# Kernel tuning notes

Hardware: AMD Instinct MI355X
Metric: run time of the kernel (lower is better)

The kernel has to match this reference:

```python
import jax, jax.numpy as jnp
import numpy as np

K_NEIGHBOURS = 16
ITERATIONS = 3
NUM_CLASSES = 20
N_POINTS = 20000


def setup_inputs() -> dict:
    key = jax.random.key(0)
    k1, k2 = jax.random.split(key)
    logits = jax.random.normal(k1, (N_POINTS, NUM_CLASSES), dtype=jnp.float32)
    coords = jax.random.uniform(k2, (N_POINTS, 3), dtype=jnp.float32)
    # nn.init.eye_ then *= -0.1
    compat_w = (-0.1 * jnp.eye(NUM_CLASSES, dtype=jnp.float32))
    return {"logits": logits, "coords": coords, "compat_w": compat_w}


def _knn_graph(coords, k):
    # torch.cdist (p=2): euclidean distances, (N, N)
    sq = jnp.sum(coords * coords, axis=-1)
    d2 = sq[:, None] + sq[None, :] - 2.0 * (coords @ coords.T)
    dists = jnp.sqrt(jnp.clip(d2, 0.0))
    # smallest-k -> top_k of negated distances
    _, idx = jax.lax.top_k(-dists, k)  # (N, k)
    return idx


def reference(logits, coords, compat_w):
    knn_idx = _knn_graph(coords, K_NEIGHBOURS)
    q = jax.nn.softmax(logits, axis=-1)
    for _ in range(ITERATIONS):
        neighbour_q = q[knn_idx]            # (N, k, K) gather
        msg = jnp.mean(neighbour_q, axis=1)  # (N, K)
        refined = logits + msg @ compat_w.T  # nn.Linear: x @ W^T
        q = jax.nn.softmax(refined, axis=-1)
    return (refined, q)
```

## Files before the change

kernel.cpp:

```cpp
#include <hip/hip_runtime.h>

#define N_PTS 20000
#define NCLS 20
#define KNN 16
#define GRID 12
#define NCELLS (GRID * GRID * GRID)
#define HCELL (1.0f / (float)GRID)
#define CAND_CAP 640
#define KEY_CAP 128
#define R_TARGET 0.0680f

__device__ __forceinline__ int cell1d(float v) {
    int c = (int)(v * (float)GRID);
    return min(max(c, 0), GRID - 1);
}

__global__ __launch_bounds__(256) void count_scan_kernel(const float* __restrict__ coords,
                                                         int* __restrict__ cellCount,
                                                         int* __restrict__ doneCtr,
                                                         int* __restrict__ cellStart,
                                                         int* __restrict__ cellCursor) {
    const int p = blockIdx.x * blockDim.x + threadIdx.x;
    if (p < N_PTS) {
        const int cx = cell1d(coords[3 * p + 0]);
        const int cy = cell1d(coords[3 * p + 1]);
        const int cz = cell1d(coords[3 * p + 2]);
        atomicAdd(&cellCount[(cz * GRID + cy) * GRID + cx], 1);
    }
    __threadfence();
    __syncthreads();
    __shared__ bool isLast;
    if (threadIdx.x == 0)
        isLast = (atomicAdd(doneCtr, 1) == (int)gridDim.x - 1);
    __syncthreads();
    if (!isLast) return;

    __shared__ int part[256];
    const int t = threadIdx.x;
    const int base = t * 7;
    int local[7];
    int s = 0;
#pragma unroll
    for (int i = 0; i < 7; ++i) {
        const int c = base + i;
        const int v = (c < NCELLS)
            ? __hip_atomic_load(&cellCount[c], __ATOMIC_RELAXED, __HIP_MEMORY_SCOPE_AGENT)
            : 0;
        local[i] = s;
        s += v;
    }
    part[t] = s;
    __syncthreads();
    for (int off = 1; off < 256; off <<= 1) {
        const int v = part[t] + ((t >= off) ? part[t - off] : 0);
        __syncthreads();
        part[t] = v;
        __syncthreads();
    }
    const int excl = (t > 0) ? part[t - 1] : 0;
#pragma unroll
    for (int i = 0; i < 7; ++i) {
        const int c = base + i;
        if (c < NCELLS) {
            cellStart[c] = excl + local[i];
            cellCursor[c] = excl + local[i];
        }
    }
    if (t == 255) cellStart[NCELLS] = part[255];
}

__global__ __launch_bounds__(256) void scatter_kernel(const float* __restrict__ coords,
                                                      const float* __restrict__ logits,
                                                      int* __restrict__ cellCursor,
                                                      float4* __restrict__ sortedPts,
                                                      int* __restrict__ orig,
                                                      float* __restrict__ ls,
                                                      float* __restrict__ q0s) {
    const int p = blockIdx.x * blockDim.x + threadIdx.x;
    if (p >= N_PTS) return;
    const float x = coords[3 * p + 0];
    const float y = coords[3 * p + 1];
    const float z = coords[3 * p + 2];
    const int c = (cell1d(z) * GRID + cell1d(y)) * GRID + cell1d(x);
    const int pos = atomicAdd(&cellCursor[c], 1);
    sortedPts[pos] = make_float4(x, y, z, __uint_as_float((unsigned)p));
    orig[pos] = p;
    const float4* l4 = (const float4*)(logits + p * NCLS);
    float v[NCLS];
#pragma unroll
    for (int u = 0; u < 5; ++u) {
        const float4 a = l4[u];
        v[4 * u + 0] = a.x; v[4 * u + 1] = a.y;
        v[4 * u + 2] = a.z; v[4 * u + 3] = a.w;
    }
    float4* d4 = (float4*)(ls + pos * NCLS);
#pragma unroll
    for (int u = 0; u < 5; ++u)
        d4[u] = make_float4(v[4 * u], v[4 * u + 1], v[4 * u + 2], v[4 * u + 3]);
    float mx = v[0];
#pragma unroll
    for (int cc = 1; cc < NCLS; ++cc) mx = fmaxf(mx, v[cc]);
    float sum = 0.f;
#pragma unroll
    for (int cc = 0; cc < NCLS; ++cc) { v[cc] = __expf(v[cc] - mx); sum += v[cc]; }
    const float inv = 1.f / sum;
    float4* q4 = (float4*)(q0s + pos * NCLS);
#pragma unroll
    for (int u = 0; u < 5; ++u)
        q4[u] = make_float4(v[4 * u] * inv, v[4 * u + 1] * inv,
                            v[4 * u + 2] * inv, v[4 * u + 3] * inv);
}

__device__ void knn_ladder(const float4* __restrict__ sortedPts,
                           const int* __restrict__ cellStart,
                           const float4 qp, const int s, int hw,
                           unsigned long long* keys, const int lane,
                           int* __restrict__ knn_out) {
    const unsigned long long laneLt = (1ull << lane) - 1ull;
    const int cx = cell1d(qp.x), cy = cell1d(qp.y), cz = cell1d(qp.z);
    float g = 0.9995f * (float)hw * HCELL;
    float tau = g * g;
    int cnt = 0;
    for (int att = 0; att < 16; ++att) {
        cnt = 0;
        const int xlo = max(cx - hw, 0), xhi = min(cx + hw, GRID - 1);
        const int ylo = max(cy - hw, 0), yhi = min(cy + hw, GRID - 1);
        const int zlo = max(cz - hw, 0), zhi = min(cz + hw, GRID - 1);
        for (int zz = zlo; zz <= zhi; ++zz) {
            for (int yy = ylo; yy <= yhi; ++yy) {
                const int rowc = (zz * GRID + yy) * GRID;
                const int beg = cellStart[rowc + xlo];
                const int end = cellStart[rowc + xhi + 1];
                for (int j0 = beg; j0 < end; j0 += 64) {
                    const int j = j0 + lane;
                    const bool jv = j < end;
                    const float4 pt = sortedPts[jv ? j : beg];
                    const float dx = pt.x - qp.x, dy = pt.y - qp.y, dz = pt.z - qp.z;
                    const float d2 = dx * dx + dy * dy + dz * dz;
                    const bool take = jv && (d2 < tau);
                    const unsigned long long mm = __ballot(take);
                    if (take) {
                        const int pos = cnt + (int)__popcll(mm & laneLt);
                        if (pos < KEY_CAP)
                            keys[pos] = (((unsigned long long)__float_as_uint(d2)) << 32) |
                                        (unsigned long long)(unsigned)j;
                    }
                    cnt += (int)__popcll(mm);
                }
            }
        }
        if (cnt >= KNN && cnt <= KEY_CAP) break;
        if (cnt < KNN) {
            if (hw < GRID - 1) { ++hw; g = 0.9995f * (float)hw * HCELL; tau = g * g; }
            else tau *= 2.5f;
        } else {
            tau *= 0.6f;
        }
    }
    const int m = min(cnt, KEY_CAP);
    const unsigned long long k0 = (lane < m) ? keys[lane] : ~0ull;
    const unsigned long long k1 = (lane + 64 < m) ? keys[lane + 64] : ~0ull;
    int r0 = 0, r1 = 0;
    for (int j = 0; j < m; ++j) {
        const unsigned long long kj = keys[j];
        r0 += (kj < k0); r1 += (kj < k1);
    }
    if (lane < m && r0 < KNN)      knn_out[s * KNN + r0] = (int)(unsigned)(k0 & 0xffffffffull);
    if (lane + 64 < m && r1 < KNN) knn_out[s * KNN + r1] = (int)(unsigned)(k1 & 0xffffffffull);
}

__global__ __launch_bounds__(256) void knn_kernel(const float4* __restrict__ sortedPts,
                                                  const int* __restrict__ cellStart,
                                                  int* __restrict__ knn_out) {
    __shared__ float4 cand[CAND_CAP];
    __shared__ unsigned long long keys[4][KEY_CAP];
    const int lane = threadIdx.x & 63;
    const int wave = threadIdx.x >> 6;
    const int c = blockIdx.x >> 1;
    const int half = blockIdx.x & 1;
    const int cz = c / (GRID * GRID);
    const int cy = (c / GRID) % GRID;
    const int cx = c % GRID;
    const int pbeg = cellStart[c];
    const int pend = cellStart[c + 1];
    const int npts = pend - pbeg;
    if (npts <= 0) return;
    const int bd = (cx == 0 || cx == GRID - 1) + (cy == 0 || cy == GRID - 1) +
                   (cz == 0 || cz == GRID - 1);
    const int hs = (bd >= 2) ? 2 : 1;
    const unsigned long long laneLt = (1ull << lane) - 1ull;

    const int xlo = max(cx - hs, 0), xhi = min(cx + hs, GRID - 1);
    const int ylo = max(cy - hs, 0), yhi = min(cy + hs, GRID - 1);
    const int zlo = max(cz - hs, 0), zhi = min(cz + hs, GRID - 1);
    const int ny = yhi - ylo + 1;
    const int nruns = (zhi - zlo + 1) * ny;

    int beg = 0, len = 0;
    if (lane < nruns) {
        const int zz = zlo + lane / ny;
        const int yy = ylo + lane % ny;
        const int rowc = (zz * GRID + yy) * GRID;
        beg = cellStart[rowc + xlo];
        len = cellStart[rowc + xhi + 1] - beg;
    }
    int off = len;
#pragma unroll
    for (int sh = 1; sh < 32; sh <<= 1) {
        const int o = __shfl_up(off, sh, 64);
        if (lane >= sh) off += o;
    }
    const int nc = __shfl(off, nruns - 1);
    off -= len;
    const int ownRun = (cz - zlo) * ny + (cy - ylo);
    const int ownOff = __shfl(off, ownRun) + (pbeg - __shfl(beg, ownRun));

    if (nc <= CAND_CAP) {
        for (int r = wave; r < nruns; r += 4) {
            const int rb = __shfl(beg, r);
            const int rl = __shfl(len, r);
            const int ro = __shfl(off, r);
            for (int i = lane; i < rl; i += 64) {
                float4 pt = sortedPts[rb + i];
                pt.w = __uint_as_float((unsigned)(rb + i));
                cand[ro + i] = pt;
            }
        }
    }
    __syncthreads();

    if (nc > CAND_CAP) {
        for (int idx = 2 * wave + half; idx < npts; idx += 8)
            knn_ladder(sortedPts, cellStart, sortedPts[pbeg + idx], pbeg + idx,
                       hs, keys[wave], lane, knn_out);
        return;
    }

    const float taumaxr = 0.9995f * (float)hs * HCELL;
    const float taumax = taumaxr * taumaxr;

    for (int idx = 2 * wave + half; idx < npts; idx += 8) {
        const int s = pbeg + idx;
        const float4 qp = cand[ownOff + idx];
        float r = R_TARGET;
        const float inv2r = 0.5f / r;
        const float fx = (fminf(qp.x + r, 1.f) - fmaxf(qp.x - r, 0.f)) * inv2r;
        const float fy = (fminf(qp.y + r, 1.f) - fmaxf(qp.y - r, 0.f)) * inv2r;
        const float fz = (fminf(qp.z + r, 1.f) - fmaxf(qp.z - r, 0.f)) * inv2r;
        const float f = fmaxf(fx * fy * fz, 0.05f);
        r = R_TARGET * __powf(f, -0.33333334f);
        float tau = fminf(r * r, taumax);
        bool triedMax = (tau >= taumax * 0.999f);

        int cnt = 0;
        bool ok = false;
        for (int att = 0; att < 5 && !ok; ++att) {
            cnt = 0;
            for (int j0 = 0; j0 < nc; j0 += 64) {
                const int j = j0 + lane;
                float d2 = 1e30f;
                unsigned pw = 0;
                if (j < nc) {
                    const float4 pt = cand[j];
                    const float dx = pt.x - qp.x, dy = pt.y - qp.y, dz = pt.z - qp.z;
                    d2 = dx * dx + dy * dy + dz * dz;
                    pw = __float_as_uint(pt.w);
                }
                const bool take = d2 < tau;
                const unsigned long long mm = __ballot(take);
                if (take) {
                    const int pos = cnt + (int)__popcll(mm & laneLt);
                    if (pos < KEY_CAP)
                        keys[wave][pos] =
                            (((unsigned long long)__float_as_uint(d2)) << 32) |
                            (unsigned long long)pw;
                }
                cnt += (int)__popcll(mm);
            }
            if (cnt >= KNN && cnt <= KEY_CAP) ok = true;
            else if (cnt < KNN) {
                if (triedMax) break;
                tau = taumax; triedMax = true;
            } else tau *= 0.6f;
        }
        if (!ok) {
            knn_ladder(sortedPts, cellStart, qp, s, hs + 1, keys[wave], lane, knn_out);
            continue;
        }
        const int m = cnt;
        const unsigned long long k0 = (lane < m) ? keys[wave][lane] : ~0ull;
        const unsigned long long k1 = (lane + 64 < m) ? keys[wave][lane + 64] : ~0ull;
        int r0 = 0, r1 = 0;
        for (int j = 0; j < m; ++j) {
            const unsigned long long kj = keys[wave][j];
            r0 += (kj < k0); r1 += (kj < k1);
        }
        if (lane < m && r0 < KNN)      knn_out[s * KNN + r0] = (int)(unsigned)(k0 & 0xffffffffull);
        if (lane + 64 < m && r1 < KNN) knn_out[s * KNN + r1] = (int)(unsigned)(k1 & 0xffffffffull);
    }
}

__global__ __launch_bounds__(256) void crf_iter_kernel(const float* __restrict__ ls,
                                                       const float* __restrict__ W,
                                                       const int* __restrict__ knn,
                                                       const float* __restrict__ qin,
                                                       float* __restrict__ qout,
                                                       const int* __restrict__ orig,
                                                       float* __restrict__ outRef,
                                                       float* __restrict__ outQ) {
    __shared__ float Ws[NCLS * NCLS];
    for (int i = threadIdx.x; i < NCLS * NCLS; i += blockDim.x) Ws[i] = W[i];
    __syncthreads();
    const int t = blockIdx.x * blockDim.x + threadIdx.x;
    const int p = t >> 2;
    const int qtr = t & 3;
    if (p >= N_PTS) return;

    float acc[NCLS];
#pragma unroll
    for (int c = 0; c < NCLS; ++c) acc[c] = 0.f;

    const int4 k4 = ((const int4*)(knn + p * KNN))[qtr];
    const int ids[4] = {k4.x, k4.y, k4.z, k4.w};
#pragma unroll
    for (int u = 0; u < 4; ++u) {
        unsigned id = (unsigned)ids[u];
        if (id >= N_PTS) id = 0;
        const float4* r4 = (const float4*)(qin + id * NCLS);
#pragma unroll
        for (int v = 0; v < 5; ++v) {
            const float4 a = r4[v];
            acc[4 * v + 0] += a.x; acc[4 * v + 1] += a.y;
            acc[4 * v + 2] += a.z; acc[4 * v + 3] += a.w;
        }
    }
#pragma unroll
    for (int c = 0; c < NCLS; ++c) {
        acc[c] += __shfl_xor(acc[c], 1, 64);
        acc[c] += __shfl_xor(acc[c], 2, 64);
        acc[c] *= (1.f / 16.f);
    }

    const int c0 = qtr * 5;
    float ref[5];
#pragma unroll
    for (int i = 0; i < 5; ++i) {
        float s = ls[p * NCLS + c0 + i];
#pragma unroll
        for (int k = 0; k < NCLS; ++k) s += acc[k] * Ws[(c0 + i) * NCLS + k];
        ref[i] = s;
    }

    float mx = ref[0];
#pragma unroll
    for (int i = 1; i < 5; ++i) mx = fmaxf(mx, ref[i]);
    mx = fmaxf(mx, __shfl_xor(mx, 1, 64));
    mx = fmaxf(mx, __shfl_xor(mx, 2, 64));
    float ex[5];
    float ps = 0.f;
#pragma unroll
    for (int i = 0; i < 5; ++i) { ex[i] = __expf(ref[i] - mx); ps += ex[i]; }
    ps += __shfl_xor(ps, 1, 64);
    ps += __shfl_xor(ps, 2, 64);
    const float inv = 1.f / ps;

    if (outRef != nullptr) {
        const int o = orig[p];
#pragma unroll
        for (int i = 0; i < 5; ++i) {
            outRef[o * NCLS + c0 + i] = ref[i];
            outQ[o * NCLS + c0 + i] = ex[i] * inv;
        }
    } else {
#pragma unroll
        for (int i = 0; i < 5; ++i) qout[p * NCLS + c0 + i] = ex[i] * inv;
    }
}

extern "C" void kernel_launch(void* const* d_in, const int* in_sizes, int n_in,
                              void* d_out, int out_size, void* d_ws, size_t ws_size,
                              hipStream_t stream) {
    const float* logits = (const float*)d_in[0];
    const float* coords = (const float*)d_in[1];
    const float* W      = (const float*)d_in[2];
    float* out = (float*)d_out;

    char* ws = (char*)d_ws;
    size_t off = 0;
    int* knn = (int*)(ws + off);              off += (size_t)N_PTS * KNN * 4;
    off = (off + 255) & ~(size_t)255;
    float* ls = (float*)(ws + off);           off += (size_t)N_PTS * NCLS * 4;
    off = (off + 255) & ~(size_t)255;
    float* q0s = (float*)(ws + off);          off += (size_t)N_PTS * NCLS * 4;
    off = (off + 255) & ~(size_t)255;
    float4* sortedPts = (float4*)(ws + off);  off += (size_t)N_PTS * 16;
    off = (off + 255) & ~(size_t)255;
    int* orig = (int*)(ws + off);             off += (size_t)N_PTS * 4;
    off = (off + 255) & ~(size_t)255;
    int* cellCount = (int*)(ws + off);        off += (size_t)(NCELLS + 1) * 4;
    int* doneCtr = cellCount + NCELLS;
    off = (off + 255) & ~(size_t)255;
    int* cellStart = (int*)(ws + off);        off += (size_t)(NCELLS + 1) * 4;
    off = (off + 255) & ~(size_t)255;
    int* cellCursor = (int*)(ws + off);
    float* q1s = out + N_PTS * NCLS;

    const int threads = 256;
    const int pblocks = (N_PTS + threads - 1) / threads;
    const int cblocks = (4 * N_PTS + threads - 1) / threads;

    hipMemsetAsync(cellCount, 0, (NCELLS + 1) * sizeof(int), stream);
    count_scan_kernel<<<pblocks, threads, 0, stream>>>(coords, cellCount, doneCtr,
                                                       cellStart, cellCursor);
    scatter_kernel<<<pblocks, threads, 0, stream>>>(coords, logits, cellCursor,
                                                    sortedPts, orig, ls, q0s);
    knn_kernel<<<NCELLS * 2, threads, 0, stream>>>(sortedPts, cellStart, knn);
    crf_iter_kernel<<<cblocks, threads, 0, stream>>>(ls, W, knn, q0s, q1s, orig,
                                                     nullptr, nullptr);
    crf_iter_kernel<<<cblocks, threads, 0, stream>>>(ls, W, knn, q1s, q0s, orig,
                                                     nullptr, nullptr);
    crf_iter_kernel<<<cblocks, threads, 0, stream>>>(ls, W, knn, q0s, nullptr, orig,
                                                     out, out + N_PTS * NCLS);
}
```

Measured before the change: 129.3 us.

## Fuse build and CRF iterations into persistent kernels with software grid barriers

After: 196.8 us. 52.3% more time.

```diff
diff --git a/kernel.cpp b/kernel.cpp
--- a/kernel.cpp
+++ b/kernel.cpp
@@ -15,17 +15,39 @@
     return min(max(c, 0), GRID - 1);
 }
 
-__global__ __launch_bounds__(256) void count_scan_kernel(const float* __restrict__ coords,
-                                                         int* __restrict__ cellCount,
-                                                         int* __restrict__ doneCtr,
-                                                         int* __restrict__ cellStart,
-                                                         int* __restrict__ cellCursor) {
+__device__ __forceinline__ void gridBarrier(int* bar, int nb) {
+    __syncthreads();
+    if (threadIdx.x == 0) {
+        __threadfence();
+        atomicAdd(bar, 1);
+        while (__hip_atomic_load(bar, __ATOMIC_RELAXED, __HIP_MEMORY_SCOPE_AGENT) < nb)
+            __builtin_amdgcn_s_sleep(2);
+        __threadfence();
+    }
+    __syncthreads();
+}
+
+__global__ __launch_bounds__(256) void build_kernel(const float* __restrict__ coords,
+                                                    const float* __restrict__ logits,
+                                                    int* __restrict__ cellCount,
+                                                    int* __restrict__ doneCtr,
+                                                    int* __restrict__ readyFlag,
+                                                    int* __restrict__ cellStart,
+                                                    int* __restrict__ cellCursor,
+                                                    float4* __restrict__ sortedPts,
+                                                    int* __restrict__ orig,
+                                                    float* __restrict__ ls,
+                                                    float* __restrict__ q0s) {
     const int p = blockIdx.x * blockDim.x + threadIdx.x;
-    if (p < N_PTS) {
-        const int cx = cell1d(coords[3 * p + 0]);
-        const int cy = cell1d(coords[3 * p + 1]);
-        const int cz = cell1d(coords[3 * p + 2]);
-        atomicAdd(&cellCount[(cz * GRID + cy) * GRID + cx], 1);
+    const bool act = (p < N_PTS);
+    float x = 0.f, y = 0.f, z = 0.f;
+    int c = 0;
+    if (act) {
+        x = coords[3 * p + 0];
+        y = coords[3 * p + 1];
+        z = coords[3 * p + 2];
+        c = (cell1d(z) * GRID + cell1d(y)) * GRID + cell1d(x);
+        atomicAdd(&cellCount[c], 1);
     }
     __threadfence();
     __syncthreads();
@@ -33,55 +55,54 @@
     if (threadIdx.x == 0)
         isLast = (atomicAdd(doneCtr, 1) == (int)gridDim.x - 1);
     __syncthreads();
-    if (!isLast) return;
-
-    __shared__ int part[256];
-    const int t = threadIdx.x;
-    const int base = t * 7;
-    int local[7];
-    int s = 0;
-#pragma unroll
-    for (int i = 0; i < 7; ++i) {
-        const int c = base + i;
-        const int v = (c < NCELLS)
-            ? __hip_atomic_load(&cellCount[c], __ATOMIC_RELAXED, __HIP_MEMORY_SCOPE_AGENT)
-            : 0;
-        local[i] = s;
-        s += v;
-    }
-    part[t] = s;
-    __syncthreads();
-    for (int off = 1; off < 256; off <<= 1) {
-        const int v = part[t] + ((t >= off) ? part[t - off] : 0);
+
+    if (isLast) {
+        __shared__ int part[256];
+        const int t = threadIdx.x;
+        const int base = t * 7;
+        int local[7];
+        int s = 0;
+#pragma unroll
+        for (int i = 0; i < 7; ++i) {
+            const int cc = base + i;
+            const int v = (cc < NCELLS)
+                ? __hip_atomic_load(&cellCount[cc], __ATOMIC_RELAXED, __HIP_MEMORY_SCOPE_AGENT)
+                : 0;
+            local[i] = s;
+            s += v;
+        }
+        part[t] = s;
         __syncthreads();
-        part[t] = v;
+        for (int off2 = 1; off2 < 256; off2 <<= 1) {
+            const int v = part[t] + ((t >= off2) ? part[t - off2] : 0);
+            __syncthreads();
+            part[t] = v;
+            __syncthreads();
+        }
+        const int excl = (t > 0) ? part[t - 1] : 0;
+#pragma unroll
+        for (int i = 0; i < 7; ++i) {
+            const int cc = base + i;
+            if (cc < NCELLS) {
+                cellStart[cc] = excl + local[i];
+                cellCursor[cc] = excl + local[i];
+            }
+        }
+        if (t == 255) cellStart[NCELLS] = part[255];
         __syncthreads();
-    }
-    const int excl = (t > 0) ? part[t - 1] : 0;
-#pragma unroll
-    for (int i = 0; i < 7; ++i) {
-        const int c = base + i;
-        if (c < NCELLS) {
-            cellStart[c] = excl + local[i];
-            cellCursor[c] = excl + local[i];
-        }
-    }
-    if (t == 255) cellStart[NCELLS] = part[255];
-}
-
-__global__ __launch_bounds__(256) void scatter_kernel(const float* __restrict__ coords,
-                                                      const float* __restrict__ logits,
-                                                      int* __restrict__ cellCursor,
-                                                      float4* __restrict__ sortedPts,
-                                                      int* __restrict__ orig,
-                                                      float* __restrict__ ls,
-                                                      float* __restrict__ q0s) {
-    const int p = blockIdx.x * blockDim.x + threadIdx.x;
-    if (p >= N_PTS) return;
-    const float x = coords[3 * p + 0];
-    const float y = coords[3 * p + 1];
-    const float z = coords[3 * p + 2];
-    const int c = (cell1d(z) * GRID + cell1d(y)) * GRID + cell1d(x);
+        if (t == 0) {
+            __threadfence();
+            __hip_atomic_store(readyFlag, 1, __ATOMIC_RELEASE, __HIP_MEMORY_SCOPE_AGENT);
+        }
+    }
+    if (threadIdx.x == 0) {
+        while (__hip_atomic_load(readyFlag, __ATOMIC_RELAXED, __HIP_MEMORY_SCOPE_AGENT) == 0)
+            __builtin_amdgcn_s_sleep(2);
+        __threadfence();
+    }
+    __syncthreads();
+    if (!act) return;
+
     const int pos = atomicAdd(&cellCursor[c], 1);
     sortedPts[pos] = make_float4(x, y, z, __uint_as_float((unsigned)p));
     orig[pos] = p;
@@ -99,10 +120,10 @@
         d4[u] = make_float4(v[4 * u], v[4 * u + 1], v[4 * u + 2], v[4 * u + 3]);
     float mx = v[0];
 #pragma unroll
-    for (int cc = 1; cc < NCLS; ++cc) mx = fmaxf(mx, v[cc]);
+    for (int cc2 = 1; cc2 < NCLS; ++cc2) mx = fmaxf(mx, v[cc2]);
     float sum = 0.f;
 #pragma unroll
-    for (int cc = 0; cc < NCLS; ++cc) { v[cc] = __expf(v[cc] - mx); sum += v[cc]; }
+    for (int cc2 = 0; cc2 < NCLS; ++cc2) { v[cc2] = __expf(v[cc2] - mx); sum += v[cc2]; }
     const float inv = 1.f / sum;
     float4* q4 = (float4*)(q0s + pos * NCLS);
 #pragma unroll
@@ -300,80 +321,91 @@
     }
 }
 
-__global__ __launch_bounds__(256) void crf_iter_kernel(const float* __restrict__ ls,
-                                                       const float* __restrict__ W,
-                                                       const int* __restrict__ knn,
-                                                       const float* __restrict__ qin,
-                                                       float* __restrict__ qout,
-                                                       const int* __restrict__ orig,
-                                                       float* __restrict__ outRef,
-                                                       float* __restrict__ outQ) {
+__global__ __launch_bounds__(256) void crf3_kernel(const float* __restrict__ ls,
+                                                   const float* __restrict__ W,
+                                                   const int* __restrict__ knn,
+                                                   float* q0s, float* q1s,
+                                                   const int* __restrict__ orig,
+                                                   float* outRef, float* outQ,
+                                                   int* bar) {
     __shared__ float Ws[NCLS * NCLS];
     for (int i = threadIdx.x; i < NCLS * NCLS; i += blockDim.x) Ws[i] = W[i];
-    __syncthreads();
     const int t = blockIdx.x * blockDim.x + threadIdx.x;
     const int p = t >> 2;
     const int qtr = t & 3;
-    if (p >= N_PTS) return;
-
-    float acc[NCLS];
-#pragma unroll
-    for (int c = 0; c < NCLS; ++c) acc[c] = 0.f;
-
-    const int4 k4 = ((const int4*)(knn + p * KNN))[qtr];
-    const int ids[4] = {k4.x, k4.y, k4.z, k4.w};
-#pragma unroll
-    for (int u = 0; u < 4; ++u) {
-        unsigned id = (unsigned)ids[u];
-        if (id >= N_PTS) id = 0;
-        const float4* r4 = (const float4*)(qin + id * NCLS);
-#pragma unroll
-        for (int v = 0; v < 5; ++v) {
-            const float4 a = r4[v];
-            acc[4 * v + 0] += a.x; acc[4 * v + 1] += a.y;
-            acc[4 * v + 2] += a.z; acc[4 * v + 3] += a.w;
-        }
-    }
-#pragma unroll
-    for (int c = 0; c < NCLS; ++c) {
-        acc[c] += __shfl_xor(acc[c], 1, 64);
-        acc[c] += __shfl_xor(acc[c], 2, 64);
-        acc[c] *= (1.f / 16.f);
-    }
-
+    const bool act = (p < N_PTS);
     const int c0 = qtr * 5;
-    float ref[5];
-#pragma unroll
-    for (int i = 0; i < 5; ++i) {
-        float s = ls[p * NCLS + c0 + i];
-#pragma unroll
-        for (int k = 0; k < NCLS; ++k) s += acc[k] * Ws[(c0 + i) * NCLS + k];
-        ref[i] = s;
-    }
-
-    float mx = ref[0];
-#pragma unroll
-    for (int i = 1; i < 5; ++i) mx = fmaxf(mx, ref[i]);
-    mx = fmaxf(mx, __shfl_xor(mx, 1, 64));
-    mx = fmaxf(mx, __shfl_xor(mx, 2, 64));
-    float ex[5];
-    float ps = 0.f;
-#pragma unroll
-    for (int i = 0; i < 5; ++i) { ex[i] = __expf(ref[i] - mx); ps += ex[i]; }
-    ps += __shfl_xor(ps, 1, 64);
-    ps += __shfl_xor(ps, 2, 64);
-    const float inv = 1.f / ps;
-
-    if (outRef != nullptr) {
-        const int o = orig[p];
-#pragma unroll
-        for (int i = 0; i < 5; ++i) {
-            outRef[o * NCLS + c0 + i] = ref[i];
-            outQ[o * NCLS + c0 + i] = ex[i] * inv;
-        }
-    } else {
-#pragma unroll
-        for (int i = 0; i < 5; ++i) qout[p * NCLS + c0 + i] = ex[i] * inv;
+
+    int4 k4 = make_int4(0, 0, 0, 0);
+    float lsr[5] = {0.f, 0.f, 0.f, 0.f, 0.f};
+    if (act) {
+        k4 = ((const int4*)(knn + p * KNN))[qtr];
+#pragma unroll
+        for (int i = 0; i < 5; ++i) lsr[i] = ls[p * NCLS + c0 + i];
+    }
+    __syncthreads();
+
+    const float* qin = q0s;
+    for (int it = 0; it < 3; ++it) {
+        if (act) {
+            float acc[NCLS];
+#pragma unroll
+            for (int c = 0; c < NCLS; ++c) acc[c] = 0.f;
+            const int ids[4] = {k4.x, k4.y, k4.z, k4.w};
+#pragma unroll
+            for (int u = 0; u < 4; ++u) {
+                unsigned id = (unsigned)ids[u];
+                if (id >= N_PTS) id = 0;
+                const float4* r4 = (const float4*)(qin + id * NCLS);
+#pragma unroll
+                for (int v = 0; v < 5; ++v) {
+                    const float4 a = r4[v];
+                    acc[4 * v + 0] += a.x; acc[4 * v + 1] += a.y;
+                    acc[4 * v + 2] += a.z; acc[4 * v + 3] += a.w;
+                }
+            }
+#pragma unroll
+            for (int c = 0; c < NCLS; ++c) {
+                acc[c] += __shfl_xor(acc[c], 1, 64);
+                acc[c] += __shfl_xor(acc[c], 2, 64);
+                acc[c] *= (1.f / 16.f);
+            }
+            float ref[5];
+#pragma unroll
+            for (int i = 0; i < 5; ++i) {
+                float s = lsr[i];
+#pragma unroll
+                for (int k = 0; k < NCLS; ++k) s += acc[k] * Ws[(c0 + i) * NCLS + k];
+                ref[i] = s;
+            }
+            float mx = ref[0];
+#pragma unroll
+            for (int i = 1; i < 5; ++i) mx = fmaxf(mx, ref[i]);
+            mx = fmaxf(mx, __shfl_xor(mx, 1, 64));
+            mx = fmaxf(mx, __shfl_xor(mx, 2, 64));
+            float ex[5];
+            float ps = 0.f;
+#pragma unroll
+            for (int i = 0; i < 5; ++i) { ex[i] = __expf(ref[i] - mx); ps += ex[i]; }
+            ps += __shfl_xor(ps, 1, 64);
+            ps += __shfl_xor(ps, 2, 64);
+            const float inv = 1.f / ps;
+
+            if (it == 2) {
+                const int o = orig[p];
+#pragma unroll
+                for (int i = 0; i < 5; ++i) {
+                    outRef[o * NCLS + c0 + i] = ref[i];
+                    outQ[o * NCLS + c0 + i] = ex[i] * inv;
+                }
+            } else {
+                float* qout = (it == 0) ? q1s : q0s;
+#pragma unroll
+                for (int i = 0; i < 5; ++i) qout[p * NCLS + c0 + i] = ex[i] * inv;
+            }
+        }
+        if (it == 0)      { gridBarrier(bar + 0, (int)gridDim.x); qin = q1s; }
+        else if (it == 1) { gridBarrier(bar + 1, (int)gridDim.x); qin = q0s; }
     }
 }
 
@@ -397,8 +429,10 @@
     off = (off + 255) & ~(size_t)255;
     int* orig = (int*)(ws + off);             off += (size_t)N_PTS * 4;
     off = (off + 255) & ~(size_t)255;
-    int* cellCount = (int*)(ws + off);        off += (size_t)(NCELLS + 1) * 4;
-    int* doneCtr = cellCount + NCELLS;
+    int* cellCount = (int*)(ws + off);        off += (size_t)(NCELLS + 4) * 4;
+    int* doneCtr   = cellCount + NCELLS;
+    int* readyFlag = cellCount + NCELLS + 1;
+    int* bar       = cellCount + NCELLS + 2;
     off = (off + 255) & ~(size_t)255;
     int* cellStart = (int*)(ws + off);        off += (size_t)(NCELLS + 1) * 4;
     off = (off + 255) & ~(size_t)255;
@@ -409,16 +443,11 @@
     const int pblocks = (N_PTS + threads - 1) / threads;
     const int cblocks = (4 * N_PTS + threads - 1) / threads;
 
-    hipMemsetAsync(cellCount, 0, (NCELLS + 1) * sizeof(int), stream);
-    count_scan_kernel<<<pblocks, threads, 0, stream>>>(coords, cellCount, doneCtr,
-                                                       cellStart, cellCursor);
-    scatter_kernel<<<pblocks, threads, 0, stream>>>(coords, logits, cellCursor,
-                                                    sortedPts, orig, ls, q0s);
+    hipMemsetAsync(cellCount, 0, (NCELLS + 4) * sizeof(int), stream);
+    build_kernel<<<pblocks, threads, 0, stream>>>(coords, logits, cellCount, doneCtr,
+                                                  readyFlag, cellStart, cellCursor,
+                                                  sortedPts, orig, ls, q0s);
     knn_kernel<<<NCELLS * 2, threads, 0, stream>>>(sortedPts, cellStart, knn);
-    crf_iter_kernel<<<cblocks, threads, 0, stream>>>(ls, W, knn, q0s, q1s, orig,
-                                                     nullptr, nullptr);
-    crf_iter_kernel<<<cblocks, threads, 0, stream>>>(ls, W, knn, q1s, q0s, orig,
-                                                     nullptr, nullptr);
-    crf_iter_kernel<<<cblocks, threads, 0, stream>>>(ls, W, knn, q0s, nullptr, orig,
-                                                     out, out + N_PTS * NCLS);
-}
+    crf3_kernel<<<cblocks, threads, 0, stream>>>(ls, W, knn, q0s, q1s, orig,
+                                                 out, out + N_PTS * NCLS, bar);
+}
```

## Replace counting-sort grid with fixed-capacity per-cell buckets and drop scan kernel

Applied to the files above, without the earlier changes.

After: 157.2 us. +21.6%, slower.

```diff
diff --git a/kernel.cpp b/kernel.cpp
--- a/kernel.cpp
+++ b/kernel.cpp
@@ -6,6 +6,7 @@
 #define GRID 12
 #define NCELLS (GRID * GRID * GRID)
 #define HCELL (1.0f / (float)GRID)
+#define CAP 64
 #define CAND_CAP 640
 #define KEY_CAP 128
 #define R_TARGET 0.0680f
@@ -15,76 +16,21 @@
     return min(max(c, 0), GRID - 1);
 }
 
-__global__ __launch_bounds__(256) void count_scan_kernel(const float* __restrict__ coords,
-                                                         int* __restrict__ cellCount,
-                                                         int* __restrict__ doneCtr,
-                                                         int* __restrict__ cellStart,
-                                                         int* __restrict__ cellCursor) {
-    const int p = blockIdx.x * blockDim.x + threadIdx.x;
-    if (p < N_PTS) {
-        const int cx = cell1d(coords[3 * p + 0]);
-        const int cy = cell1d(coords[3 * p + 1]);
-        const int cz = cell1d(coords[3 * p + 2]);
-        atomicAdd(&cellCount[(cz * GRID + cy) * GRID + cx], 1);
-    }
-    __threadfence();
-    __syncthreads();
-    __shared__ bool isLast;
-    if (threadIdx.x == 0)
-        isLast = (atomicAdd(doneCtr, 1) == (int)gridDim.x - 1);
-    __syncthreads();
-    if (!isLast) return;
-
-    __shared__ int part[256];
-    const int t = threadIdx.x;
-    const int base = t * 7;
-    int local[7];
-    int s = 0;
-#pragma unroll
-    for (int i = 0; i < 7; ++i) {
-        const int c = base + i;
-        const int v = (c < NCELLS)
-            ? __hip_atomic_load(&cellCount[c], __ATOMIC_RELAXED, __HIP_MEMORY_SCOPE_AGENT)
-            : 0;
-        local[i] = s;
-        s += v;
-    }
-    part[t] = s;
-    __syncthreads();
-    for (int off = 1; off < 256; off <<= 1) {
-        const int v = part[t] + ((t >= off) ? part[t - off] : 0);
-        __syncthreads();
-        part[t] = v;
-        __syncthreads();
-    }
-    const int excl = (t > 0) ? part[t - 1] : 0;
-#pragma unroll
-    for (int i = 0; i < 7; ++i) {
-        const int c = base + i;
-        if (c < NCELLS) {
-            cellStart[c] = excl + local[i];
-            cellCursor[c] = excl + local[i];
-        }
-    }
-    if (t == 255) cellStart[NCELLS] = part[255];
-}
-
 __global__ __launch_bounds__(256) void scatter_kernel(const float* __restrict__ coords,
                                                       const float* __restrict__ logits,
-                                                      int* __restrict__ cellCursor,
-                                                      float4* __restrict__ sortedPts,
-                                                      int* __restrict__ orig,
-                                                      float* __restrict__ ls,
-                                                      float* __restrict__ q0s) {
+                                                      int* __restrict__ cnt,
+                                                      float4* __restrict__ cellPts,
+                                                      float* __restrict__ q0) {
     const int p = blockIdx.x * blockDim.x + threadIdx.x;
     if (p >= N_PTS) return;
     const float x = coords[3 * p + 0];
     const float y = coords[3 * p + 1];
     const float z = coords[3 * p + 2];
     const int c = (cell1d(z) * GRID + cell1d(y)) * GRID + cell1d(x);
-    const int pos = atomicAdd(&cellCursor[c], 1);
-    sortedPts[pos] = make_float4(x, y, z, __uint_as_float((unsigned)p));
-    orig[pos] = p;
+    const int pos = atomicAdd(&cnt[c], 1);
+    if (pos < CAP)
+        cellPts[c * CAP + pos] = make_float4(x, y, z, __uint_as_float((unsigned)p));
+
     const float4* l4 = (const float4*)(logits + p * NCLS);
     float v[NCLS];
 #pragma unroll
@@ -93,10 +39,6 @@
         v[4 * u + 0] = a.x; v[4 * u + 1] = a.y;
         v[4 * u + 2] = a.z; v[4 * u + 3] = a.w;
     }
-    float4* d4 = (float4*)(ls + pos * NCLS);
-#pragma unroll
-    for (int u = 0; u < 5; ++u)
-        d4[u] = make_float4(v[4 * u], v[4 * u + 1], v[4 * u + 2], v[4 * u + 3]);
     float mx = v[0];
 #pragma unroll
     for (int cc = 1; cc < NCLS; ++cc) mx = fmaxf(mx, v[cc]);
@@ -104,15 +46,15 @@
 #pragma unroll
     for (int cc = 0; cc < NCLS; ++cc) { v[cc] = __expf(v[cc] - mx); sum += v[cc]; }
     const float inv = 1.f / sum;
-    float4* q4 = (float4*)(q0s + pos * NCLS);
+    float4* q4 = (float4*)(q0 + p * NCLS);
 #pragma unroll
     for (int u = 0; u < 5; ++u)
         q4[u] = make_float4(v[4 * u] * inv, v[4 * u + 1] * inv,
                             v[4 * u + 2] * inv, v[4 * u + 3] * inv);
 }
 
-__device__ void knn_ladder(const float4* __restrict__ sortedPts,
-                           const int* __restrict__ cellStart,
+__device__ void knn_ladder(const float4* __restrict__ cellPts,
+                           const int* __restrict__ cnt,
                            const float4 qp, const int s, int hw,
                            unsigned long long* keys, const int lane,
                            int* __restrict__ knn_out) {
@@ -120,57 +62,57 @@
     const int cx = cell1d(qp.x), cy = cell1d(qp.y), cz = cell1d(qp.z);
     float g = 0.9995f * (float)hw * HCELL;
     float tau = g * g;
-    int cnt = 0;
+    int m = 0;
     for (int att = 0; att < 16; ++att) {
-        cnt = 0;
+        m = 0;
         const int xlo = max(cx - hw, 0), xhi = min(cx + hw, GRID - 1);
         const int ylo = max(cy - hw, 0), yhi = min(cy + hw, GRID - 1);
         const int zlo = max(cz - hw, 0), zhi = min(cz + hw, GRID - 1);
-        for (int zz = zlo; zz <= zhi; ++zz) {
-            for (int yy = ylo; yy <= yhi; ++yy) {
-                const int rowc = (zz * GRID + yy) * GRID;
-                const int beg = cellStart[rowc + xlo];
-                const int end = cellStart[rowc + xhi + 1];
-                for (int j0 = beg; j0 < end; j0 += 64) {
-                    const int j = j0 + lane;
-                    const bool jv = j < end;
-                    const float4 pt = sortedPts[jv ? j : beg];
-                    const float dx = pt.x - qp.x, dy = pt.y - qp.y, dz = pt.z - qp.z;
-                    const float d2 = dx * dx + dy * dy + dz * dz;
-                    const bool take = jv && (d2 < tau);
-                    const unsigned long long mm = __ballot(take);
-                    if (take) {
-                        const int pos = cnt + (int)__popcll(mm & laneLt);
-                        if (pos < KEY_CAP)
-                            keys[pos] = (((unsigned long long)__float_as_uint(d2)) << 32) |
-                                        (unsigned long long)(unsigned)j;
+        for (int zz = zlo; zz <= zhi; ++zz)
+            for (int yy = ylo; yy <= yhi; ++yy)
+                for (int xx = xlo; xx <= xhi; ++xx) {
+                    const int cellc = (zz * GRID + yy) * GRID + xx;
+                    const int n = min(cnt[cellc], CAP);
+                    const int base = cellc * CAP;
+                    for (int j0 = 0; j0 < n; j0 += 64) {
+                        const int j = j0 + lane;
+                        const bool jv = j < n;
+                        const float4 pt = cellPts[base + (jv ? j : 0)];
+                        const float dx = pt.x - qp.x, dy = pt.y - qp.y, dz = pt.z - qp.z;
+                        const float d2 = dx * dx + dy * dy + dz * dz;
+                        const bool take = jv && (d2 < tau);
+                        const unsigned long long mm = __ballot(take);
+                        if (take) {
+                            const int pos = m + (int)__popcll(mm & laneLt);
+                            if (pos < KEY_CAP)
+                                keys[pos] = (((unsigned long long)__float_as_uint(d2)) << 32) |
+                                            (unsigned long long)__float_as_uint(pt.w);
+                        }
+                        m += (int)__popcll(mm);
                     }
-                    cnt += (int)__popcll(mm);
                 }
-            }
-        }
-        if (cnt >= KNN && cnt <= KEY_CAP) break;
-        if (cnt < KNN) {
+        if (m >= KNN && m <= KEY_CAP) break;
+        if (m < KNN) {
             if (hw < GRID - 1) { ++hw; g = 0.9995f * (float)hw * HCELL; tau = g * g; }
             else tau *= 2.5f;
         } else {
             tau *= 0.6f;
         }
     }
-    const int m = min(cnt, KEY_CAP);
-    const unsigned long long k0 = (lane < m) ? keys[lane] : ~0ull;
-    const unsigned long long k1 = (lane + 64 < m) ? keys[lane + 64] : ~0ull;
+    const int mm2 = min(m, KEY_CAP);
+    const unsigned long long k0 = (lane < mm2) ? keys[lane] : ~0ull;
+    const unsigned long long k1 = (lane + 64 < mm2) ? keys[lane + 64] : ~0ull;
     int r0 = 0, r1 = 0;
-    for (int j = 0; j < m; ++j) {
+    for (int j = 0; j < mm2; ++j) {
         const unsigned long long kj = keys[j];
         r0 += (kj < k0); r1 += (kj < k1);
     }
-    if (lane < m && r0 < KNN)      knn_out[s * KNN + r0] = (int)(unsigned)(k0 & 0xffffffffull);
-    if (lane + 64 < m && r1 < KNN) knn_out[s * KNN + r1] = (int)(unsigned)(k1 & 0xffffffffull);
-}
-
-__global__ __launch_bounds__(256) void knn_kernel(const float4* __restrict__ sortedPts,
-                                                  const int* __restrict__ cellStart,
+    if (lane < mm2 && r0 < KNN)      knn_out[s * KNN + r0] = (int)(unsigned)(k0 & 0xffffffffull);
+    if (lane + 64 < mm2 && r1 < KNN) knn_out[s * KNN + r1] = (int)(unsigned)(k1 & 0xffffffffull);
+}
+
+__global__ __launch_bounds__(256) void knn_kernel(const float4* __restrict__ cellPts,
+                                                  const int* __restrict__ cnt,
                                                   int* __restrict__ knn_out) {
     __shared__ float4 cand[CAND_CAP];
     __shared__ unsigned long long keys[4][KEY_CAP];
@@ -181,9 +123,7 @@
     const int cz = c / (GRID * GRID);
     const int cy = (c / GRID) % GRID;
     const int cx = c % GRID;
-    const int pbeg = cellStart[c];
-    const int pend = cellStart[c + 1];
-    const int npts = pend - pbeg;
+    const int npts = min(cnt[c], CAP);
     if (npts <= 0) return;
     const int bd = (cx == 0 || cx == GRID - 1) + (cy == 0 || cy == GRID - 1) +
                    (cz == 0 || cz == GRID - 1);
@@ -193,46 +133,47 @@
     const int xlo = max(cx - hs, 0), xhi = min(cx + hs, GRID - 1);
     const int ylo = max(cy - hs, 0), yhi = min(cy + hs, GRID - 1);
     const int zlo = max(cz - hs, 0), zhi = min(cz + hs, GRID - 1);
+    const int nx = xhi - xlo + 1;
     const int ny = yhi - ylo + 1;
-    const int nruns = (zhi - zlo + 1) * ny;
+    const int nruns = (zhi - zlo + 1) * ny * nx;
 
     int beg = 0, len = 0;
     if (lane < nruns) {
-        const int zz = zlo + lane / ny;
-        const int yy = ylo + lane % ny;
-        const int rowc = (zz * GRID + yy) * GRID;
-        beg = cellStart[rowc + xlo];
-        len = cellStart[rowc + xhi + 1] - beg;
+        const int xx = xlo + lane % nx;
+        const int yy = ylo + (lane / nx) % ny;
+        const int zz = zlo + lane / (nx * ny);
+        const int cellc = (zz * GRID + yy) * GRID + xx;
+        beg = cellc * CAP;
+        len = min(cnt[cellc], CAP);
     }
     int off = len;
 #pragma unroll
-    for (int sh = 1; sh < 32; sh <<= 1) {
+    for (int sh = 1; sh < 64; sh <<= 1) {
         const int o = __shfl_up(off, sh, 64);
         if (lane >= sh) off += o;
     }
     const int nc = __shfl(off, nruns - 1);
     off -= len;
-    const int ownRun = (cz - zlo) * ny + (cy - ylo);
-    const int ownOff = __shfl(off, ownRun) + (pbeg - __shfl(beg, ownRun));
+    const int ownRun = ((cz - zlo) * ny + (cy - ylo)) * nx + (cx - xlo);
+    const int ownOff = __shfl(off, ownRun);
 
     if (nc <= CAND_CAP) {
         for (int r = wave; r < nruns; r += 4) {
             const int rb = __shfl(beg, r);
             const int rl = __shfl(len, r);
             const int ro = __shfl(off, r);
-            for (int i = lane; i < rl; i += 64) {
-                float4 pt = sortedPts[rb + i];
-                pt.w = __uint_as_float((unsigned)(rb + i));
-                cand[ro + i] = pt;
-            }
+            for (int i = lane; i < rl; i += 64)
+                cand[ro + i] = cellPts[rb + i];
         }
     }
     __syncthreads();
 
     if (nc > CAND_CAP) {
-        for (int idx = 2 * wave + half; idx < npts; idx += 8)
-            knn_ladder(sortedPts, cellStart, sortedPts[pbeg + idx], pbeg + idx,
+        for (int idx = 2 * wave + half; idx < npts; idx += 8) {
+            const float4 qp = cellPts[c * CAP + idx];
+            knn_ladder(cellPts, cnt, qp, (int)__float_as_uint(qp.w),
                        hs, keys[wave], lane, knn_out);
+        }
         return;
     }
 
@@ -240,8 +181,8 @@
     const float taumax = taumaxr * taumaxr;
 
     for (int idx = 2 * wave + half; idx < npts; idx += 8) {
-        const int s = pbeg + idx;
         const float4 qp = cand[ownOff + idx];
+        const int s = (int)__float_as_uint(qp.w);
         float r = R_TARGET;
         const float inv2r = 0.5f / r;
         const float fx = (fminf(qp.x + r, 1.f) - fmaxf(qp.x - r, 0.f)) * inv2r;
@@ -252,10 +193,10 @@
         float tau = fminf(r * r, taumax);
         bool triedMax = (tau >= taumax * 0.999f);
 
-        int cnt = 0;
+        int m = 0;
         bool ok = false;
         for (int att = 0; att < 5 && !ok; ++att) {
-            cnt = 0;
+            m = 0;
             for (int j0 = 0; j0 < nc; j0 += 64) {
                 const int j = j0 + lane;
                 float d2 = 1e30f;
@@ -269,25 +210,24 @@
                 const bool take = d2 < tau;
                 const unsigned long long mm = __ballot(take);
                 if (take) {
-                    const int pos = cnt + (int)__popcll(mm & laneLt);
+                    const int pos = m + (int)__popcll(mm & laneLt);
                     if (pos < KEY_CAP)
                         keys[wave][pos] =
                             (((unsigned long long)__float_as_uint(d2)) << 32) |
                             (unsigned long long)pw;
                 }
-                cnt += (int)__popcll(mm);
+                m += (int)__popcll(mm);
             }
-            if (cnt >= KNN && cnt <= KEY_CAP) ok = true;
-            else if (cnt < KNN) {
+            if (m >= KNN && m <= KEY_CAP) ok = true;
+            else if (m < KNN) {
                 if (triedMax) break;
                 tau = taumax; triedMax = true;
             } else tau *= 0.6f;
         }
         if (!ok) {
-            knn_ladder(sortedPts, cellStart, qp, s, hs + 1, keys[wave], lane, knn_out);
+            knn_ladder(cellPts, cnt, qp, s, hs + 1, keys[wave], lane, knn_out);
             continue;
         }
-        const int m = cnt;
         const unsigned long long k0 = (lane < m) ? keys[wave][lane] : ~0ull;
         const unsigned long long k1 = (lane + 64 < m) ? keys[wave][lane + 64] : ~0ull;
         int r0 = 0, r1 = 0;
@@ -300,12 +240,11 @@
     }
 }
 
-__global__ __launch_bounds__(256) void crf_iter_kernel(const float* __restrict__ ls,
+__global__ __launch_bounds__(256) void crf_iter_kernel(const float* __restrict__ logits,
                                                        const float* __restrict__ W,
                                                        const int* __restrict__ knn,
                                                        const float* __restrict__ qin,
                                                        float* __restrict__ qout,
-                                                       const int* __restrict__ orig,
                                                        float* __restrict__ outRef,
                                                        float* __restrict__ outQ) {
     __shared__ float Ws[NCLS * NCLS];
@@ -345,7 +284,7 @@
     float ref[5];
 #pragma unroll
     for (int i = 0; i < 5; ++i) {
-        float s = ls[p * NCLS + c0 + i];
+        float s = logits[p * NCLS + c0 + i];
 #pragma unroll
         for (int k = 0; k < NCLS; ++k) s += acc[k] * Ws[(c0 + i) * NCLS + k];
         ref[i] = s;
@@ -365,11 +304,10 @@
     const float inv = 1.f / ps;
 
     if (outRef != nullptr) {
-        const int o = orig[p];
 #pragma unroll
         for (int i = 0; i < 5; ++i) {
-            outRef[o * NCLS + c0 + i] = ref[i];
-            outQ[o * NCLS + c0 + i] = ex[i] * inv;
+            outRef[p * NCLS + c0 + i] = ref[i];
+            outQ[p * NCLS + c0 + i] = ex[i] * inv;
         }
     } else {
 #pragma unroll
@@ -389,36 +327,24 @@
     size_t off = 0;
     int* knn = (int*)(ws + off);              off += (size_t)N_PTS * KNN * 4;
     off = (off + 255) & ~(size_t)255;
-    float* ls = (float*)(ws + off);           off += (size_t)N_PTS * NCLS * 4;
+    float* q0 = (float*)(ws + off);           off += (size_t)N_PTS * NCLS * 4;
     off = (off + 255) & ~(size_t)255;
-    float* q0s = (float*)(ws + off);          off += (size_t)N_PTS * NCLS * 4;
+    float4* cellPts = (float4*)(ws + off);    off += (size_t)NCELLS * CAP * 16;
     off = (off + 255) & ~(size_t)255;
-    float4* sortedPts = (float4*)(ws + off);  off += (size_t)N_PTS * 16;
-    off = (off + 255) & ~(size_t)255;
-    int* orig = (int*)(ws + off);             off += (size_t)N_PTS * 4;
-    off = (off + 255) & ~(size_t)255;
-    int* cellCount = (int*)(ws + off);        off += (size_t)(NCELLS + 1) * 4;
-    int* doneCtr = cellCount + NCELLS;
-    off = (off + 255) & ~(size_t)255;
-    int* cellStart = (int*)(ws + off);        off += (size_t)(NCELLS + 1) * 4;
-    off = (off + 255) & ~(size_t)255;
-    int* cellCursor = (int*)(ws + off);
-    float* q1s = out + N_PTS * NCLS;
+    int* cnt = (int*)(ws + off);              off += (size_t)NCELLS * 4;
+    float* q1 = out + N_PTS * NCLS;
 
     const int threads = 256;
     const int pblocks = (N_PTS + threads - 1) / threads;
     const int cblocks = (4 * N_PTS + threads - 1) / threads;
 
-    hipMemsetAsync(cellCount, 0, (NCELLS + 1) * sizeof(int), stream);
-    count_scan_kernel<<<pblocks, threads, 0, stream>>>(coords, cellCount, doneCtr,
-                                                       cellStart, cellCursor);
-    scatter_kernel<<<pblocks, threads, 0, stream>>>(coords, logits, cellCursor,
-                                                    sortedPts, orig, ls, q0s);
-    knn_kernel<<<NCELLS * 2, threads, 0, stream>>>(sortedPts, cellStart, knn);
-    crf_iter_kernel<<<cblocks, threads, 0, stream>>>(ls, W, knn, q0s, q1s, orig,
+    hipMemsetAsync(cnt, 0, NCELLS * sizeof(int), stream);
+    scatter_kernel<<<pblocks, threads, 0, stream>>>(coords, logits, cnt, cellPts, q0);
+    knn_kernel<<<NCELLS * 2, threads, 0, stream>>>(cellPts, cnt, knn);
+    crf_iter_kernel<<<cblocks, threads, 0, stream>>>(logits, W, knn, q0, q1,
                                                      nullptr, nullptr);
-    crf_iter_kernel<<<cblocks, threads, 0, stream>>>(ls, W, knn, q1s, q0s, orig,
+    crf_iter_kernel<<<cblocks, threads, 0, stream>>>(logits, W, knn, q1, q0,
                                                      nullptr, nullptr);
-    crf_iter_kernel<<<cblocks, threads, 0, stream>>>(ls, W, knn, q0s, nullptr, orig,
+    crf_iter_kernel<<<cblocks, threads, 0, stream>>>(logits, W, knn, q0, nullptr,
                                                      out, out + N_PTS * NCLS);
 }
```

## Defer fallback KNN ladder queries to a separate load-balanced kernel via global queue

Applied to the files above, without the earlier changes.

Measured after the change: 149.4 us. 15.6% more time.

```diff
diff --git a/kernel.cpp b/kernel.cpp
--- a/kernel.cpp
+++ b/kernel.cpp
@@ -9,6 +9,7 @@
 #define CAND_CAP 640
 #define KEY_CAP 128
 #define R_TARGET 0.0680f
+#define QCAP 8192
 
 __device__ __forceinline__ int cell1d(float v) {
     int c = (int)(v * (float)GRID);
@@ -171,7 +172,9 @@
 
 __global__ __launch_bounds__(256) void knn_kernel(const float4* __restrict__ sortedPts,
                                                   const int* __restrict__ cellStart,
-                                                  int* __restrict__ knn_out) {
+                                                  int* __restrict__ knn_out,
+                                                  int* __restrict__ qn,
+                                                  int* __restrict__ queue) {
     __shared__ float4 cand[CAND_CAP];
     __shared__ unsigned long long keys[4][KEY_CAP];
     const int lane = threadIdx.x & 63;
@@ -231,8 +234,10 @@
 
     if (nc > CAND_CAP) {
         for (int idx = 2 * wave + half; idx < npts; idx += 8)
-            knn_ladder(sortedPts, cellStart, sortedPts[pbeg + idx], pbeg + idx,
-                       hs, keys[wave], lane, knn_out);
+            if (lane == 0) {
+                const int sl = atomicAdd(qn, 1);
+                if (sl < QCAP) queue[sl] = pbeg + idx;
+            }
         return;
     }
 
@@ -284,7 +289,10 @@
             } else tau *= 0.6f;
         }
         if (!ok) {
-            knn_ladder(sortedPts, cellStart, qp, s, hs + 1, keys[wave], lane, knn_out);
+            if (lane == 0) {
+                const int sl = atomicAdd(qn, 1);
+                if (sl < QCAP) queue[sl] = s;
+            }
             continue;
         }
         const int m = cnt;
@@ -297,6 +305,28 @@
         }
         if (lane < m && r0 < KNN)      knn_out[s * KNN + r0] = (int)(unsigned)(k0 & 0xffffffffull);
         if (lane + 64 < m && r1 < KNN) knn_out[s * KNN + r1] = (int)(unsigned)(k1 & 0xffffffffull);
+    }
+}
+
+__global__ __launch_bounds__(256) void ladder_kernel(const float4* __restrict__ sortedPts,
+                                                     const int* __restrict__ cellStart,
+                                                     const int* __restrict__ qn,
+                                                     const int* __restrict__ queue,
+                                                     int* __restrict__ knn_out) {
+    __shared__ unsigned long long keys[4][KEY_CAP];
+    const int lane = threadIdx.x & 63;
+    const int wave = threadIdx.x >> 6;
+    const int gw = blockIdx.x * 4 + wave;
+    const int nw = gridDim.x * 4;
+    const int n = min(qn[0], QCAP);
+    for (int i = gw; i < n; i += nw) {
+        const int s = queue[i];
+        const float4 qp = sortedPts[s];
+        const int cx = cell1d(qp.x), cy = cell1d(qp.y), cz = cell1d(qp.z);
+        const int bd = (cx == 0 || cx == GRID - 1) + (cy == 0 || cy == GRID - 1) +
+                       (cz == 0 || cz == GRID - 1);
+        const int hs = (bd >= 2) ? 2 : 1;
+        knn_ladder(sortedPts, cellStart, qp, s, hs + 1, keys[wave], lane, knn_out);
     }
 }
 
@@ -397,24 +427,29 @@
     off = (off + 255) & ~(size_t)255;
     int* orig = (int*)(ws + off);             off += (size_t)N_PTS * 4;
     off = (off + 255) & ~(size_t)255;
-    int* cellCount = (int*)(ws + off);        off += (size_t)(NCELLS + 1) * 4;
-    int* doneCtr = cellCount + NCELLS;
+    int* cellCount = (int*)(ws + off);        off += (size_t)(NCELLS + 2) * 4;
+    int* doneCtr   = cellCount + NCELLS;
+    int* qn        = cellCount + NCELLS + 1;
     off = (off + 255) & ~(size_t)255;
     int* cellStart = (int*)(ws + off);        off += (size_t)(NCELLS + 1) * 4;
     off = (off + 255) & ~(size_t)255;
-    int* cellCursor = (int*)(ws + off);
+    int* cellCursor = (int*)(ws + off);       off += (size_t)NCELLS * 4;
+    off = (off + 255) & ~(size_t)255;
+    int* queue = (int*)(ws + off);            off += (size_t)QCAP * 4;
     float* q1s = out + N_PTS * NCLS;
 
     const int threads = 256;
     const int pblocks = (N_PTS + threads - 1) / threads;
     const int cblocks = (4 * N_PTS + threads - 1) / threads;
 
-    hipMemsetAsync(cellCount, 0, (NCELLS + 1) * sizeof(int), stream);
+    hipMemsetAsync(cellCount, 0, (NCELLS + 2) * sizeof(int), stream);
     count_scan_kernel<<<pblocks, threads, 0, stream>>>(coords, cellCount, doneCtr,
                                                        cellStart, cellCursor);
     scatter_kernel<<<pblocks, threads, 0, stream>>>(coords, logits, cellCursor,
                                                     sortedPts, orig, ls, q0s);
-    knn_kernel<<<NCELLS * 2, threads, 0, stream>>>(sortedPts, cellStart, knn);
+    knn_kernel<<<NCELLS * 2, threads, 0, stream>>>(sortedPts, cellStart, knn,
+                                                   qn, queue);
+    ladder_kernel<<<256, threads, 0, stream>>>(sortedPts, cellStart, qn, queue, knn);
     crf_iter_kernel<<<cblocks, threads, 0, stream>>>(ls, W, knn, q0s, q1s, orig,
                                                      nullptr, nullptr);
     crf_iter_kernel<<<cblocks, threads, 0, stream>>>(ls, W, knn, q1s, q0s, orig,
```
